# Optimization experiments

Measured on AMD Instinct MI355X. Metric: run time of the kernel, lower is better.

The kernel has to match this reference:

```python
import jax, jax.numpy as jnp
import numpy as np

B, DIM, H, W = 8, 64, 64, 64
N_EMBED = 512
NNZ = 4          # num_nonzero OMP iterations
REG = 1e-7       # tiny Tikhonov term for the batched normal-equation solves


def batch_omp(X, D, S):
    """Batch OMP: for each signal pick S atoms greedily and solve LS on support.
    X: [N, d] signals, D: [d, K] dictionary with unit-norm atoms.
    Returns dense sparse code [N, K] with <= S nonzeros per row.
    Mathematically equivalent to the incremental-Cholesky Batch_OMP: at each
    step we solve G_II gamma = alpha0_I on the current support I.
    """
    N, K = X.shape[0], D.shape[1]
    G = D.T @ D                 # [K, K] Gram matrix (precomputed once)
    alpha0 = X @ D              # [N, K] initial correlations D^T x
    alpha = alpha0
    idx_cols = []
    gamma = None
    idx = None
    for k in range(S):          # static small loop over sparsity level
        j = jnp.argmax(jnp.abs(alpha), axis=1)                # [N] greedy atom
        idx_cols.append(j)
        idx = jnp.stack(idx_cols, axis=1)                     # [N, k+1]
        G_sub = G[idx[:, :, None], idx[:, None, :]]           # [N, k+1, k+1]
        rhs = jnp.take_along_axis(alpha0, idx, axis=1)        # [N, k+1]
        reg = REG * jnp.eye(k + 1, dtype=G.dtype)
        gamma = jnp.linalg.solve(G_sub + reg, rhs[..., None])[..., 0]  # [N, k+1]
        # residual correlations: alpha = alpha0 - G[:, I] gamma  (G symmetric)
        alpha = alpha0 - jnp.einsum('nak,na->nk', G[idx], gamma)
    code = jnp.zeros((N, K), X.dtype).at[jnp.arange(N)[:, None], idx].set(gamma)
    return code


def setup_inputs() -> dict:
    key = jax.random.key(0)
    kx, kd = jax.random.split(key)
    x = jax.random.normal(kx, (B, DIM, H, W), dtype=jnp.float32)
    dictionary = jax.random.normal(kd, (DIM, N_EMBED), dtype=jnp.float32)
    return {"x": x, "dictionary": dictionary}


def reference(x, dictionary):
    perm = jnp.transpose(x, (0, 2, 3, 1))            # [B, H, W, C]
    flat = perm.reshape(-1, DIM)                     # [N, C], N = B*H*W
    # normalize_dict=True: atoms normalized to unit L2 norm (in-place in torch)
    Dn = dictionary / jnp.linalg.norm(dictionary, axis=0, keepdims=True)
    code = batch_omp(flat, Dn, NNZ)                  # [N, K] (torch keeps [K, N])
    quant = (code @ Dn.T).reshape(perm.shape)        # reconstruction
    diff_enc = jnp.mean((quant - perm) ** 2)
    diff_dict = diff_enc                             # backward_dict=False branch
    # straight-through: perm + (quant - perm).detach() == quant in value
    out = jnp.transpose(quant, (0, 3, 1, 2))         # [B, C, H, W]
    ids = jnp.transpose(code.reshape(B, H, W, N_EMBED), (0, 3, 1, 2))  # [B, K, H, W]
    norm_0 = jnp.sum(code != 0, axis=1).astype(jnp.float32)  # L0 per signal, [N]
    num_steps = jnp.float32(NNZ)
    mean_D = jnp.mean(jnp.abs(Dn))
    mean_Z = jnp.mean(jnp.abs(code))
    norm_Z = jnp.mean(norm_0)
    topk_num = max(1, int(norm_0.shape[0] * 0.01))   # static: 327
    top_percentile = jnp.min(jax.lax.top_k(norm_0, topk_num)[0])
    num_zeros = jnp.sum(norm_0 == 0).astype(jnp.float32)
    return (out, diff_enc, diff_dict, ids, num_steps, mean_D, mean_Z,
            norm_Z, top_percentile, num_zeros)
```

## Files before the change

### kernel.cpp

```cpp
#include <hip/hip_runtime.h>
#include <cstdint>
#include <cstddef>

#define BQ 8
#define CDIM 64
#define HQ 64
#define WQ 64
#define KDIM 512
#define N_SIG 32768
#define S_NNZ 4

#define DIFF_ENC_OFF 2097152
#define DIFF_DICT_OFF 2097153
#define IDS_OFF 2097154
#define NUM_STEPS_OFF 18874370
#define MEAN_D_OFF 18874371
#define MEAN_Z_OFF 18874372
#define NORM_Z_OFF 18874373
#define TOP_PCT_OFF 18874374
#define NUM_ZEROS_OFF 18874375

#define WS_PD 16
#define WS_DNT 24
#define WS_G 32792
#define WS_WG 294936
#define WS_WI 426008

#define DIL_OFF 4194304

typedef float v2f __attribute__((ext_vector_type(2)));

__global__ __launch_bounds__(256) void k_g(const float* __restrict__ D,
                                           float* __restrict__ G,
                                           float* __restrict__ DnT,
                                           float* __restrict__ pd,
                                           float* __restrict__ Dil,
                                           float* __restrict__ W) {
  __shared__ float Xs[64 * 64];
  __shared__ float Dns[64 * 64];
  __shared__ float partA[4][64];
  __shared__ float partB[4][64];
  __shared__ float invA[64];
  __shared__ float invB[64];
  int tid = threadIdx.x;
  int w = tid & 63, cq = tid >> 6;
  int ty = tid >> 4, tx = tid & 15;
  if (blockIdx.x == 0 && tid < 16) ((unsigned int*)W)[tid] = 0u;

  int ti = (int)blockIdx.x >> 3, tj = (int)blockIdx.x & 7;
#pragma unroll
  for (int p = 0; p < 16; ++p) {
    int c = p * 4 + cq;
    Xs[c * 64 + w] = D[(size_t)c * KDIM + ti * 64 + w];
    Dns[c * 64 + w] = D[(size_t)c * KDIM + tj * 64 + w];
  }
  __syncthreads();
  float ssA = 0.f, ssB = 0.f;
#pragma unroll
  for (int cc = 0; cc < 16; ++cc) {
    int c = cq * 16 + cc;
    float a = Xs[c * 64 + w];
    ssA = fmaf(a, a, ssA);
    float bv = Dns[c * 64 + w];
    ssB = fmaf(bv, bv, ssB);
  }
  partA[cq][w] = ssA;
  partB[cq][w] = ssB;
  __syncthreads();
  if (tid < 64) {
    invA[tid] = 1.0f / sqrtf(partA[0][tid] + partA[1][tid] + partA[2][tid] + partA[3][tid]);
    invB[tid] = 1.0f / sqrtf(partB[0][tid] + partB[1][tid] + partB[2][tid] + partB[3][tid]);
  }
  __syncthreads();
  if (ti == tj) {
    int kl = tid >> 2, cp = (tid & 3) * 16;
    float ia = invA[kl];
    int kg = ti * 64 + kl;
    int il = kg >> 3, ij = (kg >> 2) & 1, iff = kg & 3;
    float sabs = 0.f;
#pragma unroll
    for (int i = 0; i < 16; ++i) {
      int c = cp + i;
      float v = Xs[c * 64 + kl] * ia;
      DnT[(size_t)kg * CDIM + c] = v;
      Dil[((c * 2 + ij) * 64 + il) * 4 + iff] = v;
      sabs += fabsf(v);
    }
#pragma unroll
    for (int off = 32; off >= 1; off >>= 1) sabs += __shfl_xor(sabs, off);
    __syncthreads();
    if ((tid & 63) == 0) partA[0][tid >> 6] = sabs;
    __syncthreads();
    if (tid == 0) pd[ti] = partA[0][0] + partA[0][1] + partA[0][2] + partA[0][3];
  }
  v2f acc[4][2] = {};
  for (int c = 0; c < 64; ++c) {
    float4 avv = *(const float4*)&Xs[c * 64 + ty * 4];
    float av[4] = {avv.x, avv.y, avv.z, avv.w};
    float4 bv = *(const float4*)&Dns[c * 64 + tx * 4];
    v2f b0 = {bv.x, bv.y}, b1 = {bv.z, bv.w};
#pragma unroll
    for (int i = 0; i < 4; ++i) {
      v2f a2 = {av[i], av[i]};
      acc[i][0] = __builtin_elementwise_fma(a2, b0, acc[i][0]);
      acc[i][1] = __builtin_elementwise_fma(a2, b1, acc[i][1]);
    }
  }
  float sn[4] = {invB[tx * 4], invB[tx * 4 + 1], invB[tx * 4 + 2], invB[tx * 4 + 3]};
#pragma unroll
  for (int i = 0; i < 4; ++i) {
    float im = invA[ty * 4 + i];
    float4 st = make_float4(acc[i][0].x * im * sn[0], acc[i][0].y * im * sn[1],
                            acc[i][1].x * im * sn[2], acc[i][1].y * im * sn[3]);
    *(float4*)&G[(size_t)(ti * 64 + ty * 4 + i) * KDIM + tj * 64 + tx * 4] = st;
  }
}

__device__ __forceinline__ float wave_absmax_u(float m) {
#define DPP_MAX(ctrl)                                                              \
  {                                                                                \
    int t_ = __builtin_amdgcn_update_dpp(0, __float_as_int(m), (ctrl), 0xf, 0xf,   \
                                         true);                                    \
    m = fmaxf(m, __int_as_float(t_));                                              \
  }
  DPP_MAX(0x111) DPP_MAX(0x112) DPP_MAX(0x114) DPP_MAX(0x118)
  DPP_MAX(0x142) DPP_MAX(0x143)
#undef DPP_MAX
  return __int_as_float(__builtin_amdgcn_readlane(__float_as_int(m), 63));
}

template <int SZ>
__device__ __forceinline__ void solve_sz(const float (&gs)[4][4], const float (&rhs)[4],
                                         float (&gamma)[4]) {
  float M[SZ][SZ];
  float y[SZ];
  float idg[SZ];
#pragma unroll
  for (int a = 0; a < SZ; ++a) {
    y[a] = rhs[a];
#pragma unroll
    for (int b = 0; b < SZ; ++b) M[a][b] = gs[a][b] + (a == b ? 1e-7f : 0.0f);
  }
#pragma unroll
  for (int p = 0; p < SZ; ++p) {
    float ip = __builtin_amdgcn_rcpf(M[p][p]);
    idg[p] = ip;
#pragma unroll
    for (int r = p + 1; r < SZ; ++r) {
      float f = M[r][p] * ip;
#pragma unroll
      for (int c = p + 1; c < SZ; ++c) M[r][c] = fmaf(-f, M[p][c], M[r][c]);
      y[r] = fmaf(-f, y[p], y[r]);
    }
  }
#pragma unroll
  for (int r = SZ - 1; r >= 0; --r) {
    float t = y[r];
#pragma unroll
    for (int c = r + 1; c < SZ; ++c) t = fmaf(-M[r][c], gamma[c], t);
    gamma[r] = t * idg[r];
  }
}

template <int K>
__device__ __forceinline__ void omp_step2(int lane, const float* __restrict__ G,
                                          const float (&a0)[8], float (&al)[8],
                                          float (&Grow)[3][8], float (&gs)[4][4],
                                          float (&rhs)[4], int (&idx)[4],
                                          float (&gamma)[4]) {
  float mx0 = fabsf(al[0]);
  int mi = 0;
#pragma unroll
  for (int m = 1; m < 8; ++m) {
    float v = fabsf(al[m]);
    mi = (v > mx0) ? m : mi;
    mx0 = fmaxf(v, mx0);
  }
  float mx = wave_absmax_u(mx0);
  unsigned long long bm = __ballot(mx0 == mx);
  int wl = (int)__builtin_ctzll(bm);
  int mwin = __builtin_amdgcn_readlane(mi, wl);
  int sk = wl * 8 + mwin;
  idx[K] = sk;

  const float* grow_base = G + (size_t)sk * KDIM;
  if constexpr (K < 3) {
    const float4* gp = (const float4*)(grow_base + lane * 8);
    float4 r0 = gp[0], r1 = gp[1];
    Grow[K][0] = r0.x; Grow[K][1] = r0.y; Grow[K][2] = r0.z; Grow[K][3] = r0.w;
    Grow[K][4] = r1.x; Grow[K][5] = r1.y; Grow[K][6] = r1.z; Grow[K][7] = r1.w;
  }

#pragma unroll
  for (int b2 = 0; b2 < K; ++b2) {
    float v = grow_base[idx[b2]];
    gs[K][b2] = v;
    gs[b2][K] = v;
  }
  gs[K][K] = grow_base[sk];
  float pick = a0[0];
#pragma unroll
  for (int j = 1; j < 8; ++j) pick = (mwin == j) ? a0[j] : pick;
  rhs[K] = __int_as_float(__builtin_amdgcn_readlane(__float_as_int(pick), wl));

  solve_sz<K + 1>(gs, rhs, gamma);

  if constexpr (K < 3) {
#pragma unroll
    for (int m = 0; m < 8; ++m) {
      float acc2 = a0[m];
#pragma unroll
      for (int a = 0; a <= K; ++a) acc2 = fmaf(-gamma[a], Grow[a][m], acc2);
      al[m] = acc2;
    }
  }
}

__global__ __launch_bounds__(256, 2) void k_fused(const float* __restrict__ X,
                                                  const float* __restrict__ Dil,
                                                  const float* __restrict__ G,
                                                  float4* __restrict__ wg,
                                                  int4* __restrict__ wi) {
  __shared__ __align__(16) float AS[32 * 512];
  __shared__ __align__(16) float Xs[64 * 32];
  int tid = threadIdx.x;
  int lane = tid & 63;
  int wv = __builtin_amdgcn_readfirstlane(tid >> 6);
  int bid = (int)blockIdx.x;
  int mt = bid >> 1, w0 = (bid & 1) * 32;
  int b = mt >> 6, h = mt & 63;

#pragma unroll
  for (int i = 0; i < 2; ++i) {
    int fi = i * 256 + tid;
    int c = fi >> 3, w4 = (fi & 7) * 4;
    *(float4*)&Xs[c * 32 + w4] =
        *(const float4*)&X[(((size_t)b * CDIM + c) * HQ + h) * WQ + w0 + w4];
  }
  __syncthreads();

  v2f acc[8][4] = {};
  const float4* Dil4 = (const float4*)Dil;
#pragma unroll 2
  for (int c = 0; c < 64; ++c) {
    float4 g0 = Dil4[c * 128 + lane];
    float4 g1 = Dil4[c * 128 + 64 + lane];
    float4 xa = *(const float4*)&Xs[c * 32 + wv * 8];
    float4 xb = *(const float4*)&Xs[c * 32 + wv * 8 + 4];
    v2f d0 = {g0.x, g0.y}, d1 = {g0.z, g0.w}, d2 = {g1.x, g1.y}, d3 = {g1.z, g1.w};
    float xv[8] = {xa.x, xa.y, xa.z, xa.w, xb.x, xb.y, xb.z, xb.w};
#pragma unroll
    for (int s = 0; s < 8; ++s) {
      v2f xx = {xv[s], xv[s]};
      acc[s][0] = __builtin_elementwise_fma(xx, d0, acc[s][0]);
      acc[s][1] = __builtin_elementwise_fma(xx, d1, acc[s][1]);
      acc[s][2] = __builtin_elementwise_fma(xx, d2, acc[s][2]);
      acc[s][3] = __builtin_elementwise_fma(xx, d3, acc[s][3]);
    }
  }

  float4* AS4 = (float4*)AS;
#pragma unroll
  for (int s = 0; s < 8; ++s) {
    int sig = wv * 8 + s;
    AS4[sig * 128 + lane] =
        make_float4(acc[s][0].x, acc[s][0].y, acc[s][1].x, acc[s][1].y);
    AS4[sig * 128 + 64 + lane] =
        make_float4(acc[s][2].x, acc[s][2].y, acc[s][3].x, acc[s][3].y);
  }

  int nb = mt * 64 + w0 + wv * 8;
#pragma unroll 1
  for (int s = 0; s < 8; ++s) {
    int sig = wv * 8 + s;
    float4 p0 = AS4[sig * 128 + lane];
    float4 p1 = AS4[sig * 128 + 64 + lane];
    float a0[8] = {p0.x, p0.y, p0.z, p0.w, p1.x, p1.y, p1.z, p1.w};
    float al[8];
#pragma unroll
    for (int m = 0; m < 8; ++m) al[m] = a0[m];
    float Grow[3][8];
    float gs[4][4];
    float rhs[4];
    int idx[4];
    float gamma[4];
    omp_step2<0>(lane, G, a0, al, Grow, gs, rhs, idx, gamma);
    omp_step2<1>(lane, G, a0, al, Grow, gs, rhs, idx, gamma);
    omp_step2<2>(lane, G, a0, al, Grow, gs, rhs, idx, gamma);
    omp_step2<3>(lane, G, a0, al, Grow, gs, rhs, idx, gamma);
    bool k0 = (idx[0] != idx[1]) && (idx[0] != idx[2]) && (idx[0] != idx[3]);
    bool k1 = (idx[1] != idx[2]) && (idx[1] != idx[3]);
    bool k2 = (idx[2] != idx[3]);
    if (lane == 0) {
      wg[nb + s] = make_float4(k0 ? gamma[0] : 0.f, k1 ? gamma[1] : 0.f,
                               k2 ? gamma[2] : 0.f, gamma[3]);
      wi[nb + s] = make_int4(idx[0], idx[1], idx[2], idx[3]);
    }
  }
}

__global__ __launch_bounds__(256) void k_ei(const float* __restrict__ X,
                                            const float* __restrict__ DnT,
                                            const float4* __restrict__ wg,
                                            const int4* __restrict__ wi,
                                            float* __restrict__ out,
                                            double* __restrict__ accs,
                                            int* __restrict__ hist) {
  __shared__ __align__(16) int sIdx[64][4];
  __shared__ __align__(16) float sKg[64][4];
  __shared__ float q[64 * 65];
  __shared__ float red[4];
  int tid = threadIdx.x;

  if (blockIdx.x < 512) {
    int bh = blockIdx.x;
    int b = bh >> 6, h = bh & 63;
    if (tid < 64) {
      int w = tid;
      int n = bh * 64 + w;
      int4 iv = wi[n];
      float4 gv = wg[n];
      sIdx[w][0] = iv.x; sIdx[w][1] = iv.y; sIdx[w][2] = iv.z; sIdx[w][3] = iv.w;
      sKg[w][0] = gv.x; sKg[w][1] = gv.y; sKg[w][2] = gv.z; sKg[w][3] = gv.w;
      int nz = (int)(gv.x != 0.f) + (int)(gv.y != 0.f) +
               (int)(gv.z != 0.f) + (int)(gv.w != 0.f);
      float s = fabsf(gv.x) + fabsf(gv.y) + fabsf(gv.z) + fabsf(gv.w);
#pragma unroll
      for (int off = 32; off >= 1; off >>= 1) s += __shfl_xor(s, off);
#pragma unroll
      for (int v = 0; v < 5; ++v) {
        unsigned long long m = __ballot(nz == v);
        if (tid == 0) {
          int c = (int)__popcll(m);
          if (c) atomicAdd(&hist[v], c);
        }
      }
      if (tid == 0) atomicAdd(&accs[0], (double)s);
    }
    __syncthreads();

    int w2 = tid & 63, p = tid >> 6, c0 = p * 16;
    float acc[16] = {};
#pragma unroll
    for (int s = 0; s < 4; ++s) {
      int ks = sIdx[w2][s];
      float g = sKg[w2][s];
      const float4* dp = (const float4*)(DnT + (size_t)ks * CDIM + c0);
#pragma unroll
      for (int i4 = 0; i4 < 4; ++i4) {
        float4 d = dp[i4];
        acc[i4 * 4 + 0] = fmaf(g, d.x, acc[i4 * 4 + 0]);
        acc[i4 * 4 + 1] = fmaf(g, d.y, acc[i4 * 4 + 1]);
        acc[i4 * 4 + 2] = fmaf(g, d.z, acc[i4 * 4 + 2]);
        acc[i4 * 4 + 3] = fmaf(g, d.w, acc[i4 * 4 + 3]);
      }
    }
#pragma unroll
    for (int i = 0; i < 16; ++i) q[(c0 + i) * 65 + w2] = acc[i];
    __syncthreads();

    float sumsq = 0.f;
#pragma unroll
    for (int pass = 0; pass < 16; ++pass) {
      int c = pass * 4 + p;
      float qv = q[c * 65 + w2];
      size_t off = (((size_t)b * CDIM + c) * HQ + h) * WQ + w2;
      float xv = X[off];
      float d = qv - xv;
      sumsq = fmaf(d, d, sumsq);
      out[off] = qv;
    }

#pragma unroll
    for (int off = 32; off >= 1; off >>= 1) sumsq += __shfl_xor(sumsq, off);
    if ((tid & 63) == 0) red[tid >> 6] = sumsq;
    __syncthreads();
    if (tid == 0) atomicAdd(&accs[1], (double)(red[0] + red[1] + red[2] + red[3]));
  } else {
    int bid = blockIdx.x - 512;
    int bh = bid >> 2, kq = bid & 3;
    int b = bh >> 6, h = bh & 63;
    if (tid < 64) {
      int n = bh * 64 + tid;
      *(int4*)&sIdx[tid][0] = wi[n];
      *(float4*)&sKg[tid][0] = wg[n];
    }
    __syncthreads();
    int w4 = (tid & 15) * 4, kl = tid >> 4;
    int4 I0 = *(const int4*)&sIdx[w4][0];
    int4 I1 = *(const int4*)&sIdx[w4 + 1][0];
    int4 I2 = *(const int4*)&sIdx[w4 + 2][0];
    int4 I3 = *(const int4*)&sIdx[w4 + 3][0];
    float4 G0 = *(const float4*)&sKg[w4][0];
    float4 G1 = *(const float4*)&sKg[w4 + 1][0];
    float4 G2 = *(const float4*)&sKg[w4 + 2][0];
    float4 G3 = *(const float4*)&sKg[w4 + 3][0];
    float* ids = out + IDS_OFF;
    size_t base = (((size_t)b * KDIM + kq * 128 + kl) * HQ + h) * WQ + w4;
#pragma unroll
    for (int pass = 0; pass < 8; ++pass) {
      int k = kq * 128 + pass * 16 + kl;
      float4 v;
      v.x = (k == I0.w) ? G0.w : (k == I0.z) ? G0.z : (k == I0.y) ? G0.y : (k == I0.x) ? G0.x : 0.f;
      v.y = (k == I1.w) ? G1.w : (k == I1.z) ? G1.z : (k == I1.y) ? G1.y : (k == I1.x) ? G1.x : 0.f;
      v.z = (k == I2.w) ? G2.w : (k == I2.z) ? G2.z : (k == I2.y) ? G2.y : (k == I2.x) ? G2.x : 0.f;
      v.w = (k == I3.w) ? G3.w : (k == I3.z) ? G3.z : (k == I3.y) ? G3.y : (k == I3.x) ? G3.x : 0.f;
      *(float4*)&ids[base + (size_t)pass * 16 * 4096] = v;
    }
  }
}

__global__ __launch_bounds__(64) void k_final(const double* __restrict__ accs,
                                              const int* __restrict__ hist,
                                              const float* __restrict__ pd,
                                              float* __restrict__ out) {
  if (threadIdx.x == 0) {
    float sumAbsD = 0.f;
#pragma unroll
    for (int i = 0; i < 8; ++i) sumAbsD += pd[i];
    double sumAbsZ = accs[0], sumSq = accs[1];
    float diff = (float)(sumSq / 2097152.0);
    out[DIFF_ENC_OFF] = diff;
    out[DIFF_DICT_OFF] = diff;
    out[NUM_STEPS_OFF] = 4.0f;
    out[MEAN_D_OFF] = sumAbsD / 32768.0f;
    out[MEAN_Z_OFF] = (float)(sumAbsZ / 16777216.0);
    int h0 = hist[0], h1 = hist[1], h2 = hist[2], h3 = hist[3], h4 = hist[4];
    out[NORM_Z_OFF] = (float)((double)(h1 + 2 * h2 + 3 * h3 + 4 * h4) / 32768.0);
    int cum = 0, res = 0;
    for (int v = 4; v >= 0; --v) {
      cum += hist[v];
      if (cum >= 327) { res = v; break; }
    }
    out[TOP_PCT_OFF] = (float)res;
    out[NUM_ZEROS_OFF] = (float)h0;
  }
}

extern "C" void kernel_launch(void* const* d_in, const int* in_sizes, int n_in,
                              void* d_out, int out_size, void* d_ws, size_t ws_size,
                              hipStream_t stream) {
  (void)in_sizes; (void)n_in; (void)out_size; (void)ws_size;
  const float* X = (const float*)d_in[0];
  const float* D = (const float*)d_in[1];
  float* out = (float*)d_out;
  float* W = (float*)d_ws;
  double* accs = (double*)d_ws;
  int* hist = (int*)W + 4;
  float* pd = W + WS_PD;
  float* DnT = W + WS_DNT;
  float* G = W + WS_G;
  float4* wgam = (float4*)(W + WS_WG);
  int4* widx = (int4*)(W + WS_WI);
  float* Dil = out + DIL_OFF;

  hipLaunchKernelGGL(k_g, dim3(64), dim3(256), 0, stream, D, G, DnT, pd, Dil, W);
  hipLaunchKernelGGL(k_fused, dim3(1024), dim3(256), 0, stream, X, Dil, G, wgam, widx);
  hipLaunchKernelGGL(k_ei, dim3(2560), dim3(256), 0, stream, X, DnT, wgam, widx, out, accs, hist);
  hipLaunchKernelGGL(k_final, dim3(1), dim3(64), 0, stream, accs, hist, pd, out);
}
```

Baseline: 189.4 us.

## Retile fused correlation+OMP kernel to 16 signals per block with row-major dictionary

The fused kernel now handles 16 signals per block instead of 32, which halves the shared-memory footprint and doubles the grid. The occupancy hint rises from 2 to 4 blocks. The correlation GEMM is re-partitioned so each wave owns 128 atoms for all 16 signals. It reads X directly from global memory and a row-major normalized dictionary instead of staging X in LDS and using an interleaved layout. The OMP steps reload initial correlations and the rhs entry from LDS instead of keeping them in registers, trading register pressure for extra LDS reads and lower per-thread GEMM reuse.

```diff
diff --git a/kernel.cpp b/kernel.cpp
--- a/kernel.cpp
+++ b/kernel.cpp
@@ -26,7 +26,7 @@
 #define WS_WG 294936
 #define WS_WI 426008
 
-#define DIL_OFF 4194304
+#define DNR_OFF 4194304
 
 typedef float v2f __attribute__((ext_vector_type(2)));
 
@@ -34,7 +34,7 @@
                                            float* __restrict__ G,
                                            float* __restrict__ DnT,
                                            float* __restrict__ pd,
-                                           float* __restrict__ Dil,
+                                           float* __restrict__ Dnr,
                                            float* __restrict__ W) {
   __shared__ float Xs[64 * 64];
   __shared__ float Dns[64 * 64];
@@ -76,14 +76,13 @@
     int kl = tid >> 2, cp = (tid & 3) * 16;
     float ia = invA[kl];
     int kg = ti * 64 + kl;
-    int il = kg >> 3, ij = (kg >> 2) & 1, iff = kg & 3;
     float sabs = 0.f;
 #pragma unroll
     for (int i = 0; i < 16; ++i) {
       int c = cp + i;
       float v = Xs[c * 64 + kl] * ia;
       DnT[(size_t)kg * CDIM + c] = v;
-      Dil[((c * 2 + ij) * 64 + il) * 4 + iff] = v;
+      Dnr[(size_t)c * KDIM + kg] = v;
       sabs += fabsf(v);
     }
 #pragma unroll
@@ -163,11 +162,11 @@
 }
 
 template <int K>
-__device__ __forceinline__ void omp_step2(int lane, const float* __restrict__ G,
-                                          const float (&a0)[8], float (&al)[8],
-                                          float (&Grow)[3][8], float (&gs)[4][4],
-                                          float (&rhs)[4], int (&idx)[4],
-                                          float (&gamma)[4]) {
+__device__ __forceinline__ void omp_step3(int lane, const float* __restrict__ G,
+                                          const float* as_row,
+                                          float (&al)[8], float (&Grow)[3][8],
+                                          float (&gs)[4][4], float (&rhs)[4],
+                                          int (&idx)[4], float (&gamma)[4]) {
   float mx0 = fabsf(al[0]);
   int mi = 0;
 #pragma unroll
@@ -184,6 +183,11 @@
   idx[K] = sk;
 
   const float* grow_base = G + (size_t)sk * KDIM;
+  float4 p0, p1;
+  if constexpr (K < 3) {
+    p0 = *(const float4*)&as_row[lane * 8];
+    p1 = *(const float4*)&as_row[lane * 8 + 4];
+  }
   if constexpr (K < 3) {
     const float4* gp = (const float4*)(grow_base + lane * 8);
     float4 r0 = gp[0], r1 = gp[1];
@@ -198,17 +202,15 @@
     gs[b2][K] = v;
   }
   gs[K][K] = grow_base[sk];
-  float pick = a0[0];
-#pragma unroll
-  for (int j = 1; j < 8; ++j) pick = (mwin == j) ? a0[j] : pick;
-  rhs[K] = __int_as_float(__builtin_amdgcn_readlane(__float_as_int(pick), wl));
+  rhs[K] = as_row[sk];
 
   solve_sz<K + 1>(gs, rhs, gamma);
 
   if constexpr (K < 3) {
+    float a0v[8] = {p0.x, p0.y, p0.z, p0.w, p1.x, p1.y, p1.z, p1.w};
 #pragma unroll
     for (int m = 0; m < 8; ++m) {
-      float acc2 = a0[m];
+      float acc2 = a0v[m];
 #pragma unroll
       for (int a = 0; a <= K; ++a) acc2 = fmaf(-gamma[a], Grow[a][m], acc2);
       al[m] = acc2;
@@ -216,85 +218,65 @@
   }
 }
 
-__global__ __launch_bounds__(256, 2) void k_fused(const float* __restrict__ X,
-                                                  const float* __restrict__ Dil,
+__global__ __launch_bounds__(256, 4) void k_fused(const float* __restrict__ X,
+                                                  const float* __restrict__ Dnr,
                                                   const float* __restrict__ G,
                                                   float4* __restrict__ wg,
                                                   int4* __restrict__ wi) {
-  __shared__ __align__(16) float AS[32 * 512];
-  __shared__ __align__(16) float Xs[64 * 32];
+  __shared__ __align__(16) float AS[16 * 512];
   int tid = threadIdx.x;
   int lane = tid & 63;
   int wv = __builtin_amdgcn_readfirstlane(tid >> 6);
   int bid = (int)blockIdx.x;
-  int mt = bid >> 1, w0 = (bid & 1) * 32;
-  int b = mt >> 6, h = mt & 63;
-
-#pragma unroll
-  for (int i = 0; i < 2; ++i) {
-    int fi = i * 256 + tid;
-    int c = fi >> 3, w4 = (fi & 7) * 4;
-    *(float4*)&Xs[c * 32 + w4] =
-        *(const float4*)&X[(((size_t)b * CDIM + c) * HQ + h) * WQ + w0 + w4];
-  }
+  int bh = bid >> 2, w0 = (bid & 3) * 16;
+  int b = bh >> 6, h = bh & 63;
+
+  v2f acc[16] = {};
+  const v2f* dp = (const v2f*)Dnr + wv * 64 + lane;
+  const float* xbase = X + ((size_t)b * CDIM * HQ + h) * WQ + w0;
+#pragma unroll 4
+  for (int c = 0; c < 64; ++c) {
+    v2f d = dp[c * 256];
+    const float4* xp = (const float4*)(xbase + (size_t)c * (HQ * WQ));
+    float4 x0 = xp[0], x1 = xp[1], x2 = xp[2], x3 = xp[3];
+    float xv[16] = {x0.x, x0.y, x0.z, x0.w, x1.x, x1.y, x1.z, x1.w,
+                    x2.x, x2.y, x2.z, x2.w, x3.x, x3.y, x3.z, x3.w};
+#pragma unroll
+    for (int s = 0; s < 16; ++s) {
+      v2f xx = {xv[s], xv[s]};
+      acc[s] = __builtin_elementwise_fma(xx, d, acc[s]);
+    }
+  }
+
+#pragma unroll
+  for (int s = 0; s < 16; ++s)
+    *(v2f*)&AS[s * 512 + wv * 128 + lane * 2] = acc[s];
   __syncthreads();
 
-  v2f acc[8][4] = {};
-  const float4* Dil4 = (const float4*)Dil;
-#pragma unroll 2
-  for (int c = 0; c < 64; ++c) {
-    float4 g0 = Dil4[c * 128 + lane];
-    float4 g1 = Dil4[c * 128 + 64 + lane];
-    float4 xa = *(const float4*)&Xs[c * 32 + wv * 8];
-    float4 xb = *(const float4*)&Xs[c * 32 + wv * 8 + 4];
-    v2f d0 = {g0.x, g0.y}, d1 = {g0.z, g0.w}, d2 = {g1.x, g1.y}, d3 = {g1.z, g1.w};
-    float xv[8] = {xa.x, xa.y, xa.z, xa.w, xb.x, xb.y, xb.z, xb.w};
-#pragma unroll
-    for (int s = 0; s < 8; ++s) {
-      v2f xx = {xv[s], xv[s]};
-      acc[s][0] = __builtin_elementwise_fma(xx, d0, acc[s][0]);
-      acc[s][1] = __builtin_elementwise_fma(xx, d1, acc[s][1]);
-      acc[s][2] = __builtin_elementwise_fma(xx, d2, acc[s][2]);
-      acc[s][3] = __builtin_elementwise_fma(xx, d3, acc[s][3]);
-    }
-  }
-
-  float4* AS4 = (float4*)AS;
-#pragma unroll
-  for (int s = 0; s < 8; ++s) {
-    int sig = wv * 8 + s;
-    AS4[sig * 128 + lane] =
-        make_float4(acc[s][0].x, acc[s][0].y, acc[s][1].x, acc[s][1].y);
-    AS4[sig * 128 + 64 + lane] =
-        make_float4(acc[s][2].x, acc[s][2].y, acc[s][3].x, acc[s][3].y);
-  }
-
-  int nb = mt * 64 + w0 + wv * 8;
 #pragma unroll 1
-  for (int s = 0; s < 8; ++s) {
-    int sig = wv * 8 + s;
-    float4 p0 = AS4[sig * 128 + lane];
-    float4 p1 = AS4[sig * 128 + 64 + lane];
-    float a0[8] = {p0.x, p0.y, p0.z, p0.w, p1.x, p1.y, p1.z, p1.w};
-    float al[8];
-#pragma unroll
-    for (int m = 0; m < 8; ++m) al[m] = a0[m];
+  for (int s = 0; s < 4; ++s) {
+    int sb = wv * 4 + s;
+    int n = bid * 16 + sb;
+    const float* as_row = &AS[sb * 512];
+    float4 q0 = *(const float4*)&as_row[lane * 8];
+    float4 q1 = *(const float4*)&as_row[lane * 8 + 4];
+    float al[8] = {q0.x, q0.y, q0.z, q0.w, q1.x, q1.y, q1.z, q1.w};
     float Grow[3][8];
     float gs[4][4];
     float rhs[4];
     int idx[4];
     float gamma[4];
-    omp_step2<0>(lane, G, a0, al, Grow, gs, rhs, idx, gamma);
-    omp_step2<1>(lane, G, a0, al, Grow, gs, rhs, idx, gamma);
-    omp_step2<2>(lane, G, a0, al, Grow, gs, rhs, idx, gamma);
-    omp_step2<3>(lane, G, a0, al, Grow, gs, rhs, idx, gamma);
+    omp_step3<0>(lane, G, as_row, al, Grow, gs, rhs, idx, gamma);
+    omp_step3<1>(lane, G, as_row, al, Grow, gs, rhs, idx, gamma);
+    omp_step3<2>(lane, G, as_row, al, Grow, gs, rhs, idx, gamma);
+    omp_step3<3>(lane, G, as_row, al, Grow, gs, rhs, idx, gamma);
     bool k0 = (idx[0] != idx[1]) && (idx[0] != idx[2]) && (idx[0] != idx[3]);
     bool k1 = (idx[1] != idx[2]) && (idx[1] != idx[3]);
     bool k2 = (idx[2] != idx[3]);
     if (lane == 0) {
-      wg[nb + s] = make_float4(k0 ? gamma[0] : 0.f, k1 ? gamma[1] : 0.f,
-                               k2 ? gamma[2] : 0.f, gamma[3]);
-      wi[nb + s] = make_int4(idx[0], idx[1], idx[2], idx[3]);
+      wg[n] = make_float4(k0 ? gamma[0] : 0.f, k1 ? gamma[1] : 0.f,
+                          k2 ? gamma[2] : 0.f, gamma[3]);
+      wi[n] = make_int4(idx[0], idx[1], idx[2], idx[3]);
     }
   }
 }
@@ -452,10 +434,10 @@
   float* G = W + WS_G;
   float4* wgam = (float4*)(W + WS_WG);
   int4* widx = (int4*)(W + WS_WI);
-  float* Dil = out + DIL_OFF;
-
-  hipLaunchKernelGGL(k_g, dim3(64), dim3(256), 0, stream, D, G, DnT, pd, Dil, W);
-  hipLaunchKernelGGL(k_fused, dim3(1024), dim3(256), 0, stream, X, Dil, G, wgam, widx);
+  float* Dnr = out + DNR_OFF;
+
+  hipLaunchKernelGGL(k_g, dim3(64), dim3(256), 0, stream, D, G, DnT, pd, Dnr, W);
+  hipLaunchKernelGGL(k_fused, dim3(2048), dim3(256), 0, stream, X, Dnr, G, wgam, widx);
   hipLaunchKernelGGL(k_ei, dim3(2560), dim3(256), 0, stream, X, DnT, wgam, widx, out, accs, hist);
   hipLaunchKernelGGL(k_final, dim3(1), dim3(64), 0, stream, accs, hist, pd, out);
 }
```

Measured after the change: 164.6 us. 1.15x faster.
